# Optimization experiments

Measured on AMD Instinct MI355X. Metric: run time of the kernel, lower is better.

The kernel has to match this reference:

```python
import jax, jax.numpy as jnp
import numpy as np


def setup_inputs() -> dict:
    key = jax.random.key(0)
    k0, k1, k2, k3, k4 = jax.random.split(key, 5)
    K, LENGTH, D, B, MAXDEPTH = 50000, 65536, 128, 1024, 16
    weights = jax.random.normal(k0, (LENGTH, D), dtype=jnp.float32)
    x = jax.random.normal(k1, (B, D), dtype=jnp.float32)
    y = jax.random.randint(k2, (B,), 0, K, dtype=jnp.int64)
    # padded per-class paths of internal (pseudo-class) nodes; real paths index [K, LENGTH)
    path_idx = jax.random.randint(k3, (K, MAXDEPTH), 0, LENGTH, dtype=jnp.int64)
    path_len = jax.random.randint(k4, (K,), 0, MAXDEPTH, dtype=jnp.int32)
    return {"weights": weights, "x": x, "y": y, "path_idx": path_idx, "path_len": path_len}


def reference(weights, x, y, path_idx, path_len):
    # weights: [LENGTH, d]; x: [B, d]; y: [B]; path_idx: [K, Dmax]; path_len: [K]
    K, Dmax = path_idx.shape
    # mask out padded path slots (original loops over len(path)-1 real ancestors)
    mask = (jnp.arange(Dmax)[None, :] < path_len[:, None]).astype(weights.dtype)  # [K, Dmax]
    # gather ancestor rows and sum along the path; add the class's own row j
    path_sum = jnp.einsum("kpd,kp->kd", weights[path_idx], mask)  # [K, d]
    added_weights = weights[:K] + path_sum                        # [K, d]
    logits = x @ added_weights.T                                  # [B, K]
    logp = jax.nn.log_softmax(logits, axis=-1)
    loss = -jnp.take_along_axis(logp, y[:, None], axis=1).mean()  # CrossEntropyLoss (mean)
    return loss, logits, added_weights
```

## Files before the change

kernel.cpp:

```cpp
#include <hip/hip_runtime.h>
#include <math.h>

#define KCLS  50000
#define KP    50048
#define DIM   128
#define BATCH 1024
#define MAXD  16

#define NBLK_N   (KP / 128)
#define NBP      (NBLK_N * 2)
#define CLS_BLOCKS (KP / 4)
#define XB_BLOCKS  (BATCH * DIM / 1024)

typedef __attribute__((ext_vector_type(8))) short short8;
typedef __attribute__((ext_vector_type(4))) float floatx4;

__device__ __forceinline__ unsigned short f2bf(float f) {
    unsigned u = __float_as_uint(f);
    u += 0x7fffu + ((u >> 16) & 1u);
    return (unsigned short)(u >> 16);
}

__global__ __launch_bounds__(256) void aw_kernel(
    const float* __restrict__ weights, const int* __restrict__ path_idx,
    const int* __restrict__ path_len, float* __restrict__ aw,
    unsigned short* __restrict__ awb,
    const float* __restrict__ x, unsigned short* __restrict__ xb)
{
    int t = threadIdx.x;

    if (blockIdx.x >= CLS_BLOCKS) {
        int i = ((blockIdx.x - CLS_BLOCKS) * 256 + t) * 4;
        float4 v = *(const float4*)(x + i);
        ushort4 hv = { f2bf(v.x), f2bf(v.y), f2bf(v.z), f2bf(v.w) };
        *(ushort4*)(xb + i) = hv;
        return;
    }

    int w = t >> 6, lane = t & 63;
    int k = blockIdx.x * 4 + w;
    int col = lane * 2;

    if (k >= KCLS) {
        ushort2 z; z.x = 0; z.y = 0;
        *(ushort2*)(awb + (size_t)k * DIM + col) = z;
        return;
    }

    float2 acc = *(const float2*)(weights + (size_t)k * DIM + col);
    int len = path_len[k];
    const int* pp = path_idx + (size_t)k * MAXD;

    int p = 0;
    for (; p + 2 <= len; p += 2) {
        int i0 = pp[p], i1 = pp[p + 1];
        float2 a = *(const float2*)(weights + (size_t)i0 * DIM + col);
        float2 b = *(const float2*)(weights + (size_t)i1 * DIM + col);
        acc.x += a.x + b.x;
        acc.y += a.y + b.y;
    }
    if (p < len) {
        int i0 = pp[p];
        float2 a = *(const float2*)(weights + (size_t)i0 * DIM + col);
        acc.x += a.x;
        acc.y += a.y;
    }

    *(float2*)(aw + (size_t)k * DIM + col) = acc;
    ushort2 hv; hv.x = f2bf(acc.x); hv.y = f2bf(acc.y);
    *(ushort2*)(awb + (size_t)k * DIM + col) = hv;
}

template<bool PART>
__global__ __launch_bounds__(256) void gemm_kernel(
    const unsigned short* __restrict__ Xb,
    const unsigned short* __restrict__ Wb,
    float* __restrict__ logits,
    float2* __restrict__ part)
{
    int tid = threadIdx.x;
    int wave = tid >> 6, lane = tid & 63;
    int r = lane & 15, quad = lane >> 4;
    int m0 = blockIdx.y * 128 + (wave >> 1) * 64;
    int n0 = blockIdx.x * 128 + (wave & 1) * 64;

    const unsigned short* ap = Xb + (size_t)(m0 + r) * DIM + quad * 8;
    const unsigned short* bp = Wb + (size_t)(n0 + r) * DIM + quad * 8;

    floatx4 acc[4][4];
    #pragma unroll
    for (int i = 0; i < 4; ++i)
        #pragma unroll
        for (int j = 0; j < 4; ++j)
            acc[i][j] = (floatx4){0.f, 0.f, 0.f, 0.f};

    #pragma unroll
    for (int kk = 0; kk < 4; ++kk) {
        short8 a[4], b[4];
        #pragma unroll
        for (int i = 0; i < 4; ++i)
            a[i] = *(const short8*)(ap + (size_t)(i * 16) * DIM + kk * 32);
        #pragma unroll
        for (int j = 0; j < 4; ++j)
            b[j] = *(const short8*)(bp + (size_t)(j * 16) * DIM + kk * 32);
        #pragma unroll
        for (int i = 0; i < 4; ++i)
            #pragma unroll
            for (int j = 0; j < 4; ++j)
                acc[i][j] = __builtin_amdgcn_mfma_f32_16x16x32_bf16(
                    a[i], b[j], acc[i][j], 0, 0, 0);
    }

    #pragma unroll
    for (int i = 0; i < 4; ++i) {
        int mrow = m0 + i * 16 + quad * 4;

        #pragma unroll
        for (int j = 0; j < 4; ++j) {
            int col = n0 + j * 16 + r;
            if (col < KCLS) {
                float* cp = logits + (size_t)mrow * KCLS + col;
                #pragma unroll
                for (int reg = 0; reg < 4; ++reg)
                    cp[(size_t)reg * KCLS] = acc[i][j][reg];
            }
        }

        if constexpr (PART) {
            #pragma unroll
            for (int reg = 0; reg < 4; ++reg) {
                float v[4];
                #pragma unroll
                for (int j = 0; j < 4; ++j) {
                    int col = n0 + j * 16 + r;
                    v[j] = (col < KCLS) ? acc[i][j][reg] : -INFINITY;
                }
                float mx = fmaxf(fmaxf(v[0], v[1]), fmaxf(v[2], v[3]));
                #pragma unroll
                for (int off = 8; off; off >>= 1)
                    mx = fmaxf(mx, __shfl_xor(mx, off));
                float s = __expf(v[0] - mx) + __expf(v[1] - mx)
                        + __expf(v[2] - mx) + __expf(v[3] - mx);
                #pragma unroll
                for (int off = 8; off; off >>= 1)
                    s += __shfl_xor(s, off);
                if (r == 0)
                    part[(size_t)(mrow + reg) * NBP + blockIdx.x * 2 + (wave & 1)]
                        = make_float2(mx, s);
            }
        }
    }
}

__global__ __launch_bounds__(256) void lsereduce_kernel(
    const float2* __restrict__ part, const float* __restrict__ logits,
    const int* __restrict__ y, float* __restrict__ loss)
{
    int b = blockIdx.x * 4 + (threadIdx.x >> 6);
    int lane = threadIdx.x & 63;
    const float2* pr = part + (size_t)b * NBP;

    float m = -INFINITY, s = 0.f;
    for (int i = lane; i < NBP; i += 64) {
        float2 pv = pr[i];
        if (pv.x > m) {
            s = s * __expf(m - pv.x) + pv.y;
            m = pv.x;
        } else {
            s += pv.y * __expf(pv.x - m);
        }
    }
    #pragma unroll
    for (int off = 32; off; off >>= 1) {
        float m2 = __shfl_xor(m, off);
        float s2 = __shfl_xor(s, off);
        float M = fmaxf(m, m2);
        s = s * __expf(m - M) + s2 * __expf(m2 - M);
        m = M;
    }
    if (lane == 0) {
        float lse = m + __logf(s);
        float ly = logits[(size_t)b * KCLS + y[b]];
        atomicAdd(loss, (lse - ly) * (1.0f / BATCH));
    }
}

__global__ __launch_bounds__(256) void lse_kernel(
    const float* __restrict__ logits, const int* __restrict__ y,
    float* __restrict__ loss)
{
    int b = blockIdx.x;
    const float* row = logits + (size_t)b * KCLS;
    float m = -INFINITY, s = 0.f;

    auto upd = [&](float v) {
        if (v <= m) {
            s += __expf(v - m);
        } else {
            s = s * __expf(m - v) + 1.f;
            m = v;
        }
    };

    if (threadIdx.x < 3) upd(row[threadIdx.x]);
    const float4* rv = (const float4*)(row + 3);
    for (int i = threadIdx.x; i < 12499; i += 256) {
        float4 v = rv[i];
        upd(v.x); upd(v.y); upd(v.z); upd(v.w);
    }
    if (threadIdx.x == 3) upd(row[49999]);

    #pragma unroll
    for (int off = 32; off > 0; off >>= 1) {
        float m2 = __shfl_down(m, off);
        float s2 = __shfl_down(s, off);
        float M = fmaxf(m, m2);
        s = s * __expf(m - M) + s2 * __expf(m2 - M);
        m = M;
    }
    __shared__ float sm[4], ss[4];
    int w = threadIdx.x >> 6, l = threadIdx.x & 63;
    if (l == 0) { sm[w] = m; ss[w] = s; }
    __syncthreads();
    if (threadIdx.x == 0) {
        m = sm[0]; s = ss[0];
        #pragma unroll
        for (int i = 1; i < 4; ++i) {
            float M = fmaxf(m, sm[i]);
            s = s * __expf(m - M) + ss[i] * __expf(sm[i] - M);
            m = M;
        }
        float lse = m + __logf(s);
        float ly = row[y[b]];
        atomicAdd(loss, (lse - ly) * (1.0f / BATCH));
    }
}

extern "C" void kernel_launch(void* const* d_in, const int* in_sizes, int n_in,
                              void* d_out, int out_size, void* d_ws, size_t ws_size,
                              hipStream_t stream)
{
    const float* weights  = (const float*)d_in[0];
    const float* x        = (const float*)d_in[1];
    const int*   y        = (const int*)d_in[2];
    const int*   path_idx = (const int*)d_in[3];
    const int*   path_len = (const int*)d_in[4];

    float* out    = (float*)d_out;
    float* loss   = out;
    float* logits = out + 1;
    float* aw     = out + 1 + (size_t)BATCH * KCLS;

    size_t awb_sz  = (size_t)KP * DIM * sizeof(unsigned short);
    size_t xb_sz   = (size_t)BATCH * DIM * sizeof(unsigned short);
    size_t part_sz = (size_t)BATCH * NBP * sizeof(float2);

    unsigned short* awb = (unsigned short*)d_ws;
    unsigned short* xb  = awb + (size_t)KP * DIM;
    float2* part = (float2*)((char*)d_ws + awb_sz + xb_sz);
    bool fused = ws_size >= awb_sz + xb_sz + part_sz;

    hipMemsetAsync(loss, 0, sizeof(float), stream);

    aw_kernel<<<CLS_BLOCKS + XB_BLOCKS, 256, 0, stream>>>(
        weights, path_idx, path_len, aw, awb, x, xb);

    if (fused) {
        gemm_kernel<true><<<dim3(NBLK_N, BATCH / 128), 256, 0, stream>>>(
            xb, awb, logits, part);
        lsereduce_kernel<<<BATCH / 4, 256, 0, stream>>>(part, logits, y, loss);
    } else {
        gemm_kernel<false><<<dim3(NBLK_N, BATCH / 128), 256, 0, stream>>>(
            xb, awb, logits, nullptr);
        lse_kernel<<<BATCH, 256, 0, stream>>>(logits, y, loss);
    }
}
```

Baseline: 400.3 us.

## Swap GEMM operands for vectorized nontemporal logit stores and unroll path gather

The GEMM now puts class weights in the MFMA A operand and batch rows in B, so each lane holds four consecutive class columns of one batch row. That allows 16-byte nontemporal stores of the large logits matrix instead of scattered scalar stores. The grid is reordered so batch tiles vary fastest, which keeps the same weight tile shared across neighbouring blocks, and the partial softmax reduction is rewritten to match the new register layout with fewer shuffles. The path-gather loop is also unrolled by four to issue more independent loads per iteration.

```diff
diff --git a/kernel.cpp b/kernel.cpp
--- a/kernel.cpp
+++ b/kernel.cpp
@@ -52,14 +52,16 @@
     const int* pp = path_idx + (size_t)k * MAXD;
 
     int p = 0;
-    for (; p + 2 <= len; p += 2) {
-        int i0 = pp[p], i1 = pp[p + 1];
+    for (; p + 4 <= len; p += 4) {
+        int i0 = pp[p], i1 = pp[p + 1], i2 = pp[p + 2], i3 = pp[p + 3];
         float2 a = *(const float2*)(weights + (size_t)i0 * DIM + col);
         float2 b = *(const float2*)(weights + (size_t)i1 * DIM + col);
-        acc.x += a.x + b.x;
-        acc.y += a.y + b.y;
-    }
-    if (p < len) {
+        float2 c = *(const float2*)(weights + (size_t)i2 * DIM + col);
+        float2 d = *(const float2*)(weights + (size_t)i3 * DIM + col);
+        acc.x += (a.x + b.x) + (c.x + d.x);
+        acc.y += (a.y + b.y) + (c.y + d.y);
+    }
+    for (; p < len; ++p) {
         int i0 = pp[p];
         float2 a = *(const float2*)(weights + (size_t)i0 * DIM + col);
         acc.x += a.x;
@@ -81,11 +83,11 @@
     int tid = threadIdx.x;
     int wave = tid >> 6, lane = tid & 63;
     int r = lane & 15, quad = lane >> 4;
-    int m0 = blockIdx.y * 128 + (wave >> 1) * 64;
-    int n0 = blockIdx.x * 128 + (wave & 1) * 64;
-
-    const unsigned short* ap = Xb + (size_t)(m0 + r) * DIM + quad * 8;
-    const unsigned short* bp = Wb + (size_t)(n0 + r) * DIM + quad * 8;
+    int m0 = blockIdx.x * 128 + (wave >> 1) * 64;
+    int n0 = blockIdx.y * 128 + (wave & 1) * 64;
+
+    const unsigned short* wp = Wb + (size_t)(n0 + r) * DIM + quad * 8;
+    const unsigned short* xp = Xb + (size_t)(m0 + r) * DIM + quad * 8;
 
     floatx4 acc[4][4];
     #pragma unroll
@@ -99,10 +101,10 @@
         short8 a[4], b[4];
         #pragma unroll
         for (int i = 0; i < 4; ++i)
-            a[i] = *(const short8*)(ap + (size_t)(i * 16) * DIM + kk * 32);
+            a[i] = *(const short8*)(wp + (size_t)(i * 16) * DIM + kk * 32);
         #pragma unroll
         for (int j = 0; j < 4; ++j)
-            b[j] = *(const short8*)(bp + (size_t)(j * 16) * DIM + kk * 32);
+            b[j] = *(const short8*)(xp + (size_t)(j * 16) * DIM + kk * 32);
         #pragma unroll
         for (int i = 0; i < 4; ++i)
             #pragma unroll
@@ -112,42 +114,45 @@
     }
 
     #pragma unroll
-    for (int i = 0; i < 4; ++i) {
-        int mrow = m0 + i * 16 + quad * 4;
-
-        #pragma unroll
-        for (int j = 0; j < 4; ++j) {
-            int col = n0 + j * 16 + r;
-            if (col < KCLS) {
-                float* cp = logits + (size_t)mrow * KCLS + col;
+    for (int j = 0; j < 4; ++j) {
+        int mrow = m0 + j * 16 + r;
+        float* rowp = logits + (size_t)mrow * KCLS;
+
+        #pragma unroll
+        for (int i = 0; i < 4; ++i) {
+            int nb = n0 + i * 16 + quad * 4;
+            if (nb < KCLS)
+                __builtin_nontemporal_store(acc[i][j], (floatx4*)(rowp + nb));
+        }
+
+        if constexpr (PART) {
+            float mx = -INFINITY;
+            #pragma unroll
+            for (int i = 0; i < 4; ++i) {
+                bool ok = (n0 + i * 16 + quad * 4) < KCLS;
                 #pragma unroll
-                for (int reg = 0; reg < 4; ++reg)
-                    cp[(size_t)reg * KCLS] = acc[i][j][reg];
+                for (int reg = 0; reg < 4; ++reg) {
+                    float v = ok ? acc[i][j][reg] : -INFINITY;
+                    mx = fmaxf(mx, v);
+                }
             }
-        }
-
-        if constexpr (PART) {
+            mx = fmaxf(mx, __shfl_xor(mx, 16));
+            mx = fmaxf(mx, __shfl_xor(mx, 32));
+            float s = 0.f;
             #pragma unroll
-            for (int reg = 0; reg < 4; ++reg) {
-                float v[4];
+            for (int i = 0; i < 4; ++i) {
+                bool ok = (n0 + i * 16 + quad * 4) < KCLS;
                 #pragma unroll
-                for (int j = 0; j < 4; ++j) {
-                    int col = n0 + j * 16 + r;
-                    v[j] = (col < KCLS) ? acc[i][j][reg] : -INFINITY;
+                for (int reg = 0; reg < 4; ++reg) {
+                    float v = ok ? acc[i][j][reg] : -INFINITY;
+                    s += __expf(v - mx);
                 }
-                float mx = fmaxf(fmaxf(v[0], v[1]), fmaxf(v[2], v[3]));
-                #pragma unroll
-                for (int off = 8; off; off >>= 1)
-                    mx = fmaxf(mx, __shfl_xor(mx, off));
-                float s = __expf(v[0] - mx) + __expf(v[1] - mx)
-                        + __expf(v[2] - mx) + __expf(v[3] - mx);
-                #pragma unroll
-                for (int off = 8; off; off >>= 1)
-                    s += __shfl_xor(s, off);
-                if (r == 0)
-                    part[(size_t)(mrow + reg) * NBP + blockIdx.x * 2 + (wave & 1)]
-                        = make_float2(mx, s);
             }
+            s += __shfl_xor(s, 16);
+            s += __shfl_xor(s, 32);
+            if (quad == 0)
+                part[(size_t)mrow * NBP + blockIdx.y * 2 + (wave & 1)]
+                    = make_float2(mx, s);
         }
     }
 }
@@ -260,17 +265,17 @@
     float2* part = (float2*)((char*)d_ws + awb_sz + xb_sz);
     bool fused = ws_size >= awb_sz + xb_sz + part_sz;
 
-    hipMemsetAsync(loss, 0, sizeof(float), stream);
+    (void)hipMemsetAsync(loss, 0, sizeof(float), stream);
 
     aw_kernel<<<CLS_BLOCKS + XB_BLOCKS, 256, 0, stream>>>(
         weights, path_idx, path_len, aw, awb, x, xb);
 
     if (fused) {
-        gemm_kernel<true><<<dim3(NBLK_N, BATCH / 128), 256, 0, stream>>>(
+        gemm_kernel<true><<<dim3(BATCH / 128, NBLK_N), 256, 0, stream>>>(
             xb, awb, logits, part);
         lsereduce_kernel<<<BATCH / 4, 256, 0, stream>>>(part, logits, y, loss);
     } else {
-        gemm_kernel<false><<<dim3(NBLK_N, BATCH / 128), 256, 0, stream>>>(
+        gemm_kernel<false><<<dim3(BATCH / 128, NBLK_N), 256, 0, stream>>>(
             xb, awb, logits, nullptr);
         lse_kernel<<<BATCH, 256, 0, stream>>>(logits, y, loss);
     }
```

Measured after the change: 481.6 us. 1.2x slower.
